# Kernel tuning notes

Hardware: AMD Instinct MI355X
Metric: run time of the kernel (lower is better)

Reference implementation:

```python
import jax, jax.numpy as jnp
import numpy as np

BATCH = 4
N_MELS, T_LEN, PATCH = 128, 512, 16
D_MODEL, D_INNER, D_STATE, DT_RANK, D_CONV = 512, 1024, 16, 32, 4
DEPTH, N_CLASSES = 4, 10


def _silu(x):
    return x * jax.nn.sigmoid(x)


def _ln(x, w, b):
    m = x.mean(-1, keepdims=True)
    v = ((x - m) ** 2).mean(-1, keepdims=True)
    return (x - m) * jax.lax.rsqrt(v + 1e-5) * w + b


def _causal_conv(x, w, b):
    # x: (B, L, D); w: (D, K) depthwise causal conv (mamba conv1d)
    K, L = w.shape[-1], x.shape[1]
    xp = jnp.pad(x, ((0, 0), (K - 1, 0), (0, 0)))
    y = sum(xp[:, k:k + L, :] * w[:, k] for k in range(K))
    return y + b


def _ssm(xc, conv_w, conv_b, xproj_w, dtproj_w, dtproj_b, A_log, Dp):
    # One directional selective scan (mamba S6).
    u = _silu(_causal_conv(xc, conv_w, conv_b))              # (B,L,Di)
    xdbl = jnp.einsum('bld,ed->ble', u, xproj_w)             # (B,L,dt_rank+2S)
    dtr, Bm, Cm = jnp.split(xdbl, [DT_RANK, DT_RANK + D_STATE], axis=-1)
    dt = jax.nn.softplus(jnp.einsum('blr,dr->bld', dtr, dtproj_w) + dtproj_b)
    A = -jnp.exp(A_log)                                      # (Di,S)
    dA = jnp.exp(dt[..., None] * A)                          # (B,L,Di,S)
    dBu = (dt * u)[..., None] * Bm[:, :, None, :]            # (B,L,Di,S)

    def comb(e1, e2):
        a1, b1 = e1
        a2, b2 = e2
        return a1 * a2, a2 * b1 + b2

    _, h = jax.lax.associative_scan(comb, (dA, dBu), axis=1)  # parallel linear recurrence
    return jnp.einsum('blds,bls->bld', h, Cm) + u * Dp


def _forward(x, patch_w, patch_b, in_proj_w, conv_w_f, conv_b_f, conv_w_b, conv_b_b,
             xproj_w_f, xproj_w_b, dtproj_w_f, dtproj_b_f, dtproj_w_b, dtproj_b_b,
             A_log_f, A_log_b, D_f, D_b, out_proj_w, norm_w, norm_b,
             normf_w, normf_b, ln_w, ln_b, fc1_w, fc1_b, fc2_w, fc2_b):
    B = x.shape[0]
    # Patch embed: conv with kernel == stride -> reshape + einsum
    xp = x.reshape(B, 1, N_MELS // PATCH, PATCH, T_LEN // PATCH, PATCH)
    tok = jnp.einsum('bchpwq,dcpq->bhwd', xp, patch_w) + patch_b
    h = tok.reshape(B, -1, D_MODEL)                           # (B, 256, D)
    for i in range(DEPTH):
        xn = _ln(h, norm_w[i], norm_b[i])
        xz = jnp.einsum('bld,ed->ble', xn, in_proj_w[i])
        xc, z = jnp.split(xz, 2, axis=-1)
        y_f = _ssm(xc, conv_w_f[i], conv_b_f[i], xproj_w_f[i],
                   dtproj_w_f[i], dtproj_b_f[i], A_log_f[i], D_f[i])
        y_b = jnp.flip(_ssm(jnp.flip(xc, 1), conv_w_b[i], conv_b_b[i], xproj_w_b[i],
                            dtproj_w_b[i], dtproj_b_b[i], A_log_b[i], D_b[i]), 1)
        y = (y_f + y_b) * _silu(z)                            # bimamba v2: fwd + flipped bwd, gated
        h = h + jnp.einsum('bld,ed->ble', y, out_proj_w[i])
    h = _ln(h, normf_w, normf_b)
    feat = h.mean(axis=1)                                     # pooled features (B, D)
    c = _ln(feat, ln_w, ln_b)
    c = jnp.maximum(c @ fc1_w.T + fc1_b, 0.0)
    return c @ fc2_w.T + fc2_b


def setup_inputs() -> dict:
    ks = iter(jax.random.split(jax.random.key(0), 64))

    def rn(shape, s=0.02):
        return jax.random.normal(next(ks), shape, jnp.float32) * s

    inp = {}
    inp['x'] = jax.random.normal(next(ks), (BATCH, 1, N_MELS, T_LEN), jnp.float32)
    inp['patch_w'] = rn((D_MODEL, 1, PATCH, PATCH))
    inp['patch_b'] = jnp.zeros((D_MODEL,), jnp.float32)
    inp['in_proj_w'] = rn((DEPTH, 2 * D_INNER, D_MODEL))
    A_init = jnp.log(jnp.tile(jnp.arange(1, D_STATE + 1, dtype=jnp.float32), (DEPTH, D_INNER, 1)))
    for sfx in ('f', 'b'):
        inp[f'conv_w_{sfx}'] = rn((DEPTH, D_INNER, D_CONV), 0.2)
        inp[f'conv_b_{sfx}'] = jnp.zeros((DEPTH, D_INNER), jnp.float32)
        inp[f'xproj_w_{sfx}'] = rn((DEPTH, DT_RANK + 2 * D_STATE, D_INNER))
        inp[f'dtproj_w_{sfx}'] = rn((DEPTH, D_INNER, DT_RANK), 0.1)
        inp[f'dtproj_b_{sfx}'] = jnp.full((DEPTH, D_INNER), -4.6, jnp.float32)  # softplus -> dt ~ 0.01
        inp[f'A_log_{sfx}'] = A_init
        inp[f'D_{sfx}'] = jnp.ones((DEPTH, D_INNER), jnp.float32)
    inp['out_proj_w'] = rn((DEPTH, D_MODEL, D_INNER))
    inp['norm_w'] = jnp.ones((DEPTH, D_MODEL), jnp.float32)
    inp['norm_b'] = jnp.zeros((DEPTH, D_MODEL), jnp.float32)
    inp['normf_w'] = jnp.ones((D_MODEL,), jnp.float32)
    inp['normf_b'] = jnp.zeros((D_MODEL,), jnp.float32)
    inp['ln_w'] = jnp.ones((D_MODEL,), jnp.float32)
    inp['ln_b'] = jnp.zeros((D_MODEL,), jnp.float32)
    inp['fc1_w'] = rn((512, D_MODEL))
    inp['fc1_b'] = jnp.zeros((512,), jnp.float32)
    inp['fc2_w'] = rn((N_CLASSES, 512))
    inp['fc2_b'] = jnp.zeros((N_CLASSES,), jnp.float32)
    return inp


def reference(x, patch_w, patch_b, in_proj_w, conv_w_f, conv_b_f, conv_w_b, conv_b_b,
              xproj_w_f, xproj_w_b, dtproj_w_f, dtproj_b_f, dtproj_w_b, dtproj_b_b,
              A_log_f, A_log_b, D_f, D_b, out_proj_w, norm_w, norm_b,
              normf_w, normf_b, ln_w, ln_b, fc1_w, fc1_b, fc2_w, fc2_b):
    return _forward(x, patch_w, patch_b, in_proj_w, conv_w_f, conv_b_f, conv_w_b, conv_b_b,
                    xproj_w_f, xproj_w_b, dtproj_w_f, dtproj_b_f, dtproj_w_b, dtproj_b_b,
                    A_log_f, A_log_b, D_f, D_b, out_proj_w, norm_w, norm_b,
                    normf_w, normf_b, ln_w, ln_b, fc1_w, fc1_b, fc2_w, fc2_b)
```

## Files before the change

kernel.cpp:

```cpp
#include <hip/hip_runtime.h>


#define BB 4
#define LL 256
#define DM 512
#define DI 1024
#define LDST 40

typedef unsigned short u16;
typedef unsigned int u32;
typedef __attribute__((ext_vector_type(8))) short s8v;
typedef __attribute__((ext_vector_type(4))) float f4v;

__device__ __forceinline__ float silu_f(float x){ return x/(1.f+__expf(-x)); }
__device__ __forceinline__ float b2f(u16 u){
  union { u32 i; float f; } v; v.i = ((u32)u) << 16; return v.f;
}
__device__ __forceinline__ u16 f2bf(float f){
  union { float f; u32 u; } v; v.f = f;
  u32 r = (v.u + 0x7fffu + ((v.u >> 16) & 1u)) >> 16;
  return (u16)r;
}

__device__ __forceinline__ float row_sum16(float p){
  union { float f; int i; } v, r;
  v.f = p;
  r.i = __builtin_amdgcn_update_dpp(0, v.i, 0x111, 0xF, 0xF, true); v.f += r.f;
  r.i = __builtin_amdgcn_update_dpp(0, v.i, 0x112, 0xF, 0xF, true); v.f += r.f;
  r.i = __builtin_amdgcn_update_dpp(0, v.i, 0x114, 0xF, 0xF, true); v.f += r.f;
  r.i = __builtin_amdgcn_update_dpp(0, v.i, 0x118, 0xF, 0xF, true); v.f += r.f;
  return v.f;
}

__device__ __forceinline__ void block_reduce2(float& a, float& b, float* sc, int nw){
  int lane = threadIdx.x & 63, wid = threadIdx.x >> 6;
#pragma unroll
  for (int o = 32; o > 0; o >>= 1){
    a += __shfl_down(a, o, 64);
    b += __shfl_down(b, o, 64);
  }
  if (lane == 0){ sc[wid*2] = a; sc[wid*2+1] = b; }
  __syncthreads();
  float ta = 0.f, tb = 0.f;
  for (int i = 0; i < nw; ++i){ ta += sc[i*2]; tb += sc[i*2+1]; }
  a = ta; b = tb;
}

__global__ __launch_bounds__(256) void convert_w(const float* __restrict__ inW,
    const float* __restrict__ outW, u16* __restrict__ inHi, u16* __restrict__ inLo,
    u16* __restrict__ outHi, u16* __restrict__ outLo){
  int idx = blockIdx.x*256 + threadIdx.x;
  const float4* src; ushort4* dh; ushort4* dl;
  if (idx < 262144){
    src = (const float4*)inW + idx;
    dh = (ushort4*)inHi + idx; dl = (ushort4*)inLo + idx;
  } else {
    int j = idx - 262144;
    src = (const float4*)outW + j;
    dh = (ushort4*)outHi + j; dl = (ushort4*)outLo + j;
  }
  float4 v = *src;
  ushort4 h, l;
  h.x = f2bf(v.x); l.x = f2bf(v.x - b2f(h.x));
  h.y = f2bf(v.y); l.y = f2bf(v.y - b2f(h.y));
  h.z = f2bf(v.z); l.z = f2bf(v.z - b2f(h.z));
  h.w = f2bf(v.w); l.w = f2bf(v.w - b2f(h.w));
  *dh = h; *dl = l;
}

__global__ __launch_bounds__(256) void patch_embed(const float* __restrict__ x,
    const float* __restrict__ pw, const float* __restrict__ pb, float* __restrict__ h){
  __shared__ float xs[8*256];
  int blk = blockIdx.x;
  int b = blk >> 6, ph = (blk >> 3) & 7, pg = (blk >> 1) & 3, dh = blk & 1;
  int t = threadIdx.x;
  for (int idx = t; idx < 2048; idx += 256){
    int j = idx >> 8, pix = idx & 255, p = pix >> 4, q = pix & 15;
    xs[idx] = x[(size_t)(b*128 + ph*16 + p)*512 + pg*128 + j*16 + q];
  }
  __syncthreads();
  int d = dh*256 + t;
  float acc[8] = {};
  const float* wr = pw + (size_t)d*256;
  for (int i = 0; i < 256; i += 8){
    float4 w0 = *(const float4*)(wr + i);
    float4 w1 = *(const float4*)(wr + i + 4);
    float wf[8] = {w0.x,w0.y,w0.z,w0.w,w1.x,w1.y,w1.z,w1.w};
#pragma unroll
    for (int j = 0; j < 8; ++j){
#pragma unroll
      for (int jj = 0; jj < 8; ++jj)
        acc[j] = fmaf(xs[j*256 + i + jj], wf[jj], acc[j]);
    }
  }
  float bias = pb[d];
#pragma unroll
  for (int j = 0; j < 8; ++j)
    h[(size_t)(b*256 + ph*32 + pg*8 + j)*512 + d] = acc[j] + bias;
}

__global__ __launch_bounds__(256) void prep_ln(const float* __restrict__ x,
    const float* __restrict__ w, const float* __restrict__ bias, int wOff,
    u16* __restrict__ hiO, u16* __restrict__ loO){
  __shared__ float sc[8];
  int row = blockIdx.x, t = threadIdx.x;
  const float* xr = x + (size_t)row*DM;
  float v0 = xr[t], v1 = xr[t + 256];
  float s = v0 + v1, ss = v0*v0 + v1*v1;
  block_reduce2(s, ss, sc, 4);
  float mean = s * (1.f/512.f);
  float var = ss * (1.f/512.f) - mean*mean;
  float inv = rsqrtf(var + 1e-5f);
  float o0 = (v0 - mean)*inv*w[wOff + t]       + bias[wOff + t];
  float o1 = (v1 - mean)*inv*w[wOff + t + 256] + bias[wOff + t + 256];
  u16 h0 = f2bf(o0), h1 = f2bf(o1);
  hiO[(size_t)row*DM + t]       = h0;
  hiO[(size_t)row*DM + t + 256] = h1;
  loO[(size_t)row*DM + t]       = f2bf(o0 - b2f(h0));
  loO[(size_t)row*DM + t + 256] = f2bf(o1 - b2f(h1));
}

__global__ __launch_bounds__(256) void prep_gate(const float* __restrict__ ybuf,
    const float* __restrict__ xz, u16* __restrict__ gHi, u16* __restrict__ gLo){
  int row = blockIdx.x, t = threadIdx.x;
  int c = t*4;
  float4 yf = *(const float4*)(ybuf + (size_t)row*DI + c);
  float4 yb = *(const float4*)(ybuf + 1048576 + (size_t)row*DI + c);
  float4 zv = *(const float4*)(xz + (size_t)row*2048 + 1024 + c);
  float g0 = (yf.x + yb.x)*silu_f(zv.x);
  float g1 = (yf.y + yb.y)*silu_f(zv.y);
  float g2 = (yf.z + yb.z)*silu_f(zv.z);
  float g3 = (yf.w + yb.w)*silu_f(zv.w);
  ushort4 h, l;
  h.x = f2bf(g0); l.x = f2bf(g0 - b2f(h.x));
  h.y = f2bf(g1); l.y = f2bf(g1 - b2f(h.y));
  h.z = f2bf(g2); l.z = f2bf(g2 - b2f(h.z));
  h.w = f2bf(g3); l.w = f2bf(g3 - b2f(h.w));
  *(ushort4*)(gHi + (size_t)row*DI + c) = h;
  *(ushort4*)(gLo + (size_t)row*DI + c) = l;
}

__global__ __launch_bounds__(256) void gemm_bf16(const u16* __restrict__ Ahi_g,
    const u16* __restrict__ Alo_g, int As, const u16* __restrict__ Bhi_g,
    const u16* __restrict__ Blo_g, int Bs, float* __restrict__ C, int Cs,
    int K, int addFlag){
  __shared__ __align__(16) u16 Ah[64*LDST], Al[64*LDST], Bh[64*LDST], Bl[64*LDST];
  int bm = blockIdx.y*64, bn = blockIdx.x*64;
  int t = threadIdx.x;
  int sr = t >> 2, sc8 = (t & 3)*8;
  int lane = t & 63, wv = t >> 6, ml = lane & 15, quad = lane >> 4;
  int mq = wv >> 1, nq = wv & 1;
  f4v acc[2][2] = {};
  for (int k0 = 0; k0 < K; k0 += 32){
    *(uint4*)&Ah[sr*LDST + sc8] = *(const uint4*)(Ahi_g + (size_t)(bm + sr)*As + k0 + sc8);
    *(uint4*)&Al[sr*LDST + sc8] = *(const uint4*)(Alo_g + (size_t)(bm + sr)*As + k0 + sc8);
    *(uint4*)&Bh[sr*LDST + sc8] = *(const uint4*)(Bhi_g + (size_t)(bn + sr)*Bs + k0 + sc8);
    *(uint4*)&Bl[sr*LDST + sc8] = *(const uint4*)(Blo_g + (size_t)(bn + sr)*Bs + k0 + sc8);
    __syncthreads();
    s8v ah[2], al2[2], bh2[2], bl2[2];
#pragma unroll
    for (int mt = 0; mt < 2; ++mt){
      int row = mq*32 + mt*16 + ml;
      ah[mt]  = *(s8v*)&Ah[row*LDST + quad*8];
      al2[mt] = *(s8v*)&Al[row*LDST + quad*8];
    }
#pragma unroll
    for (int nt = 0; nt < 2; ++nt){
      int col = nq*32 + nt*16 + ml;
      bh2[nt] = *(s8v*)&Bh[col*LDST + quad*8];
      bl2[nt] = *(s8v*)&Bl[col*LDST + quad*8];
    }
#pragma unroll
    for (int mt = 0; mt < 2; ++mt)
#pragma unroll
      for (int nt = 0; nt < 2; ++nt){
        acc[mt][nt] = __builtin_amdgcn_mfma_f32_16x16x32_bf16(ah[mt],  bh2[nt], acc[mt][nt], 0, 0, 0);
        acc[mt][nt] = __builtin_amdgcn_mfma_f32_16x16x32_bf16(al2[mt], bh2[nt], acc[mt][nt], 0, 0, 0);
        acc[mt][nt] = __builtin_amdgcn_mfma_f32_16x16x32_bf16(ah[mt],  bl2[nt], acc[mt][nt], 0, 0, 0);
      }
    __syncthreads();
  }
#pragma unroll
  for (int mt = 0; mt < 2; ++mt)
#pragma unroll
    for (int nt = 0; nt < 2; ++nt)
#pragma unroll
      for (int r = 0; r < 4; ++r){
        float* cp = C + (size_t)(bm + mq*32 + mt*16 + quad*4 + r)*Cs +
                    bn + nq*32 + nt*16 + ml;
        if (addFlag) *cp += acc[mt][nt][r];
        else         *cp  = acc[mt][nt][r];
      }
}

__global__ __launch_bounds__(256) void fused_cxd(const float* __restrict__ xz,
    const float* __restrict__ cwF, const float* __restrict__ cbF,
    const float* __restrict__ cwB, const float* __restrict__ cbB,
    const float* __restrict__ xwF, const float* __restrict__ xwB,
    const float* __restrict__ dtwF, const float* __restrict__ dtbF,
    const float* __restrict__ dtwB, const float* __restrict__ dtbB,
    int cwOff, int cbOff, int xwOff, int dtwOff, int dtbOff,
    float* __restrict__ u, float* __restrict__ xdbl, float* __restrict__ dtout){
  __shared__ float us[4*1024];
  __shared__ float part[16*64];
  __shared__ float dtr[4*32];
  int blk = blockIdx.x;
  int dir = blk >> 8, rem = blk & 255, b = rem >> 6, lg = rem & 63;
  int l0 = lg*4;
  const float* cw  = dir ? cwB  : cwF;
  const float* cb  = dir ? cbB  : cbF;
  const float* xw  = dir ? xwB  : xwF;
  const float* dtw = dir ? dtwB : dtwF;
  const float* dtb = dir ? dtbB : dtbF;
  int t = threadIdx.x;
  int rbase = (dir*BB + b)*LL;
  for (int dd = 0; dd < 4; ++dd){
    int d = t + dd*256;
    float4 w4 = *(const float4*)(cw + cwOff + d*4);
    float wf[4] = {w4.x, w4.y, w4.z, w4.w};
    float bias = cb[cbOff + d];
#pragma unroll
    for (int r = 0; r < 4; ++r){
      int l = l0 + r;
      float acc = bias;
#pragma unroll
      for (int k = 0; k < 4; ++k){
        int li = l + k - 3;
        if (li >= 0){
          int sl = dir ? (LL-1-li) : li;
          acc = fmaf(xz[(size_t)(b*LL + sl)*2048 + d], wf[k], acc);
        }
      }
      float uval = silu_f(acc);
      us[r*1024 + d] = uval;
      u[(size_t)(rbase + l)*DI + d] = uval;
    }
  }
  __syncthreads();
  {
    int e = t & 63, pr = t >> 6;
    float accs[4] = {};
    const float* wr = xw + xwOff + (size_t)e*1024 + pr*256;
    for (int i = 0; i < 256; i += 8){
      float4 w0 = *(const float4*)(wr + i);
      float4 w1 = *(const float4*)(wr + i + 4);
      float wf[8] = {w0.x,w0.y,w0.z,w0.w,w1.x,w1.y,w1.z,w1.w};
#pragma unroll
      for (int r = 0; r < 4; ++r){
        const float* ub = us + r*1024 + pr*256 + i;
#pragma unroll
        for (int j = 0; j < 8; ++j)
          accs[r] = fmaf(ub[j], wf[j], accs[r]);
      }
    }
#pragma unroll
    for (int r = 0; r < 4; ++r) part[(pr*4 + r)*64 + e] = accs[r];
  }
  __syncthreads();
  {
    int r = t >> 6, e = t & 63;
    float v = part[(0*4+r)*64+e] + part[(1*4+r)*64+e] +
              part[(2*4+r)*64+e] + part[(3*4+r)*64+e];
    xdbl[(size_t)(rbase + l0 + r)*64 + e] = v;
    if (e < 32) dtr[r*32 + e] = v;
  }
  __syncthreads();
  for (int dd = 0; dd < 4; ++dd){
    int d = t + dd*256;
    float bias = dtb[dtbOff + d];
    float accs[4] = {bias, bias, bias, bias};
    const float* wr = dtw + dtwOff + (size_t)d*32;
    for (int i = 0; i < 32; i += 8){
      float4 w0 = *(const float4*)(wr + i);
      float4 w1 = *(const float4*)(wr + i + 4);
      float wf[8] = {w0.x,w0.y,w0.z,w0.w,w1.x,w1.y,w1.z,w1.w};
#pragma unroll
      for (int r = 0; r < 4; ++r)
#pragma unroll
        for (int j = 0; j < 8; ++j)
          accs[r] = fmaf(dtr[r*32 + i + j], wf[j], accs[r]);
    }
#pragma unroll
    for (int r = 0; r < 4; ++r){
      float sv = accs[r];
      dtout[(size_t)(rbase + l0 + r)*DI + d] = (sv > 15.f) ? sv : log1pf(__expf(sv));
    }
  }
}

__global__ __launch_bounds__(256) void scan_coal(const float* __restrict__ dt,
    const float* __restrict__ u, const float* __restrict__ xd,
    const float* __restrict__ AlogF, const float* __restrict__ AlogB,
    const float* __restrict__ DF, const float* __restrict__ DB,
    int aOff, int dOff, float* __restrict__ y){
  __shared__ __align__(16) float dtuT[16][516];
  __shared__ __align__(16) float BCT[16][516];
  __shared__ __align__(16) float ytile[128][16];
  int blk = blockIdx.x;
  int dir = blk >> 8, b = (blk >> 6) & 3, dg = blk & 63;
  int t = threadIdx.x;
  int rbase = (dir*BB + b)*LL;
  const float* Alog = dir ? AlogB : AlogF;
  const float* Dpt  = dir ? DB : DF;
  {
    int q = t & 3, lb = t >> 2;
    for (int pass = 0; pass < 4; ++pass){
      int l = pass*64 + lb;
      float4 dv = *(const float4*)(dt + (size_t)(rbase + l)*DI + dg*16 + q*4);
      float4 uv = *(const float4*)(u  + (size_t)(rbase + l)*DI + dg*16 + q*4);
      float2 p0 = {dv.x, uv.x}, p1 = {dv.y, uv.y}, p2 = {dv.z, uv.z}, p3 = {dv.w, uv.w};
      *(float2*)&dtuT[q*4+0][l*2] = p0;
      *(float2*)&dtuT[q*4+1][l*2] = p1;
      *(float2*)&dtuT[q*4+2][l*2] = p2;
      *(float2*)&dtuT[q*4+3][l*2] = p3;
    }
  }
  {
    int h8 = t & 7, lb = t >> 3;
    for (int pass = 0; pass < 8; ++pass){
      int l = pass*32 + lb;
      float4 v = *(const float4*)(xd + (size_t)(rbase + l)*64 + 32 + h8*4);
      if (h8 < 4){
        int s0 = h8*4;
        BCT[s0+0][l*2] = v.x; BCT[s0+1][l*2] = v.y;
        BCT[s0+2][l*2] = v.z; BCT[s0+3][l*2] = v.w;
      } else {
        int s0 = (h8-4)*4;
        BCT[s0+0][l*2+1] = v.x; BCT[s0+1][l*2+1] = v.y;
        BCT[s0+2][l*2+1] = v.z; BCT[s0+3][l*2+1] = v.w;
      }
    }
  }
  int s = t & 15, dl = t >> 4;
  float Av = -__expf(Alog[aOff + dg*256 + t]);
  float Dp = Dpt[dOff + dg*16 + dl];
  __syncthreads();
  float h = 0.f;
  for (int half = 0; half < 2; ++half){
    for (int l0 = half*128; l0 < half*128 + 128; l0 += 4){
      float4 du01 = *(const float4*)&dtuT[dl][l0*2];
      float4 du23 = *(const float4*)&dtuT[dl][l0*2 + 4];
      float4 bc01 = *(const float4*)&BCT[s][l0*2];
      float4 bc23 = *(const float4*)&BCT[s][l0*2 + 4];
      float dtv[4] = {du01.x, du01.z, du23.x, du23.z};
      float uv[4]  = {du01.y, du01.w, du23.y, du23.w};
      float Bv[4]  = {bc01.x, bc01.z, bc23.x, bc23.z};
      float Cv[4]  = {bc01.y, bc01.w, bc23.y, bc23.w};
#pragma unroll
      for (int i = 0; i < 4; ++i){
        float a = __expf(dtv[i] * Av);
        h = fmaf(a, h, dtv[i]*uv[i]*Bv[i]);
        float p = h * Cv[i];
        float sum = row_sum16(p);
        if (s == 15){
          int lr = (l0 + i) & 127;
          ytile[lr][dl] = fmaf(uv[i], Dp, sum);
        }
      }
    }
    __syncthreads();
    {
      int d4 = t & 3, lh = t >> 2;
      for (int pass = 0; pass < 2; ++pass){
        int lr = pass*64 + lh;
        int l = half*128 + lr;
        int lo = dir ? (255 - l) : l;
        float4 vv = *(const float4*)&ytile[lr][d4*4];
        *(float4*)(y + (size_t)(rbase + lo)*DI + dg*16 + d4*4) = vv;
      }
    }
    __syncthreads();
  }
}

__global__ __launch_bounds__(256) void ln_kernel(const float* __restrict__ x,
    const float* __restrict__ w, const float* __restrict__ bias,
    float* __restrict__ y){
  __shared__ float sc[8];
  int row = blockIdx.x, t = threadIdx.x;
  const float* xr = x + (size_t)row*DM;
  float v0 = xr[t], v1 = xr[t + 256];
  float s = v0 + v1, ss = v0*v0 + v1*v1;
  block_reduce2(s, ss, sc, 4);
  float mean = s * (1.f/512.f);
  float var = ss * (1.f/512.f) - mean*mean;
  float inv = rsqrtf(var + 1e-5f);
  float* yr = y + (size_t)row*DM;
  yr[t]       = (v0 - mean)*inv*w[t]       + bias[t];
  yr[t + 256] = (v1 - mean)*inv*w[t + 256] + bias[t + 256];
}

__global__ __launch_bounds__(256) void pool_kernel(const float* __restrict__ hn,
    float* __restrict__ feat){
  __shared__ float part[4][64];
  int b = blockIdx.x >> 3, dg = blockIdx.x & 7;
  int t = threadIdx.x, dl = t & 63, lq = t >> 6;
  const float* p = hn + (size_t)(b*256 + lq*64)*512 + dg*64 + dl;
  float s = 0.f;
#pragma unroll 4
  for (int i = 0; i < 64; ++i) s += p[(size_t)i*512];
  part[lq][dl] = s;
  __syncthreads();
  if (t < 64)
    feat[b*512 + dg*64 + t] =
        (part[0][t] + part[1][t] + part[2][t] + part[3][t]) * (1.f/256.f);
}

__global__ __launch_bounds__(512) void head_kernel(const float* __restrict__ feat,
    const float* __restrict__ lnw, const float* __restrict__ lnb,
    const float* __restrict__ fc1w, const float* __restrict__ fc1b,
    const float* __restrict__ fc2w, const float* __restrict__ fc2b,
    float* __restrict__ out){
  __shared__ float sc[16];
  __shared__ float cbuf[512];
  __shared__ float rbuf[512];
  int b = blockIdx.x, t = threadIdx.x;
  float v = feat[b*512 + t];
  float s = v, ss = v*v;
  block_reduce2(s, ss, sc, 8);
  float mean = s * (1.f/512.f);
  float var = ss * (1.f/512.f) - mean*mean;
  float inv = rsqrtf(var + 1e-5f);
  cbuf[t] = (v - mean)*inv*lnw[t] + lnb[t];
  __syncthreads();
  float a = fc1b[t];
  const float* w1 = fc1w + (size_t)t*512;
  for (int i = 0; i < 512; i += 8){
    float4 w0 = *(const float4*)(w1 + i);
    float4 w4 = *(const float4*)(w1 + i + 4);
    float wf[8] = {w0.x,w0.y,w0.z,w0.w,w4.x,w4.y,w4.z,w4.w};
#pragma unroll
    for (int j = 0; j < 8; ++j) a = fmaf(cbuf[i + j], wf[j], a);
  }
  rbuf[t] = fmaxf(a, 0.f);
  __syncthreads();
  if (t < 10){
    float a2 = fc2b[t];
    const float* w2 = fc2w + (size_t)t*512;
    for (int i = 0; i < 512; ++i) a2 = fmaf(rbuf[i], w2[i], a2);
    out[b*10 + t] = a2;
  }
}

extern "C" void kernel_launch(void* const* d_in, const int* in_sizes, int n_in,
                              void* d_out, int out_size, void* d_ws, size_t ws_size,
                              hipStream_t stream) {
  (void)in_sizes; (void)n_in; (void)out_size; (void)ws_size;
  const float* x          = (const float*)d_in[0];
  const float* patch_w    = (const float*)d_in[1];
  const float* patch_b    = (const float*)d_in[2];
  const float* in_proj_w  = (const float*)d_in[3];
  const float* conv_w_f   = (const float*)d_in[4];
  const float* conv_b_f   = (const float*)d_in[5];
  const float* xproj_w_f  = (const float*)d_in[6];
  const float* dtproj_w_f = (const float*)d_in[7];
  const float* dtproj_b_f = (const float*)d_in[8];
  const float* A_log_f    = (const float*)d_in[9];
  const float* D_f        = (const float*)d_in[10];
  const float* conv_w_b   = (const float*)d_in[11];
  const float* conv_b_b   = (const float*)d_in[12];
  const float* xproj_w_b  = (const float*)d_in[13];
  const float* dtproj_w_b = (const float*)d_in[14];
  const float* dtproj_b_b = (const float*)d_in[15];
  const float* A_log_b    = (const float*)d_in[16];
  const float* D_b        = (const float*)d_in[17];
  const float* out_proj_w = (const float*)d_in[18];
  const float* norm_w     = (const float*)d_in[19];
  const float* norm_b     = (const float*)d_in[20];
  const float* normf_w    = (const float*)d_in[21];
  const float* normf_b    = (const float*)d_in[22];
  const float* ln_w       = (const float*)d_in[23];
  const float* ln_b       = (const float*)d_in[24];
  const float* fc1_w      = (const float*)d_in[25];
  const float* fc1_b      = (const float*)d_in[26];
  const float* fc2_w      = (const float*)d_in[27];
  const float* fc2_b      = (const float*)d_in[28];

  float* ws   = (float*)d_ws;
  float* hbuf = ws;
  float* xz   = ws + 524288;
  float* ubuf = ws + 2621440;
  float* xdbl = ws + 4718592;
  float* dtb  = ws + 4849664;
  float* ybuf = ws + 6946816;
  float* hn   = ws + 9043968;
  u16*   inHi = (u16*)(ws + 9568256);
  u16*   inLo = (u16*)(ws + 10092544);
  u16*   outHi= (u16*)(ws + 10616832);
  u16*   outLo= (u16*)(ws + 10878976);
  float* feat = ws + 11141120;
  u16*   xnHi = (u16*)hn;
  u16*   xnLo = (u16*)(ws + 9043968 + 262144);
  u16*   gHi  = (u16*)ubuf;
  u16*   gLo  = (u16*)(ws + 2621440 + 524288);

  patch_embed<<<256, 256, 0, stream>>>(x, patch_w, patch_b, hbuf);
  for (int i = 0; i < 4; ++i){
    convert_w<<<1536, 256, 0, stream>>>(in_proj_w + (size_t)i*1048576,
                                        out_proj_w + (size_t)i*524288,
                                        inHi, inLo, outHi, outLo);
    prep_ln<<<1024, 256, 0, stream>>>(hbuf, norm_w, norm_b, i*512, xnHi, xnLo);
    gemm_bf16<<<dim3(32, 16), 256, 0, stream>>>(
        xnHi, xnLo, 512, inHi, inLo, 512, xz, 2048, 512, 0);
    fused_cxd<<<512, 256, 0, stream>>>(
        xz, conv_w_f, conv_b_f, conv_w_b, conv_b_b, xproj_w_f, xproj_w_b,
        dtproj_w_f, dtproj_b_f, dtproj_w_b, dtproj_b_b,
        i*4096, i*1024, i*65536, i*32768, i*1024, ubuf, xdbl, dtb);
    scan_coal<<<512, 256, 0, stream>>>(
        dtb, ubuf, xdbl, A_log_f, A_log_b, D_f, D_b, i*16384, i*1024, ybuf);
    prep_gate<<<1024, 256, 0, stream>>>(ybuf, xz, gHi, gLo);
    gemm_bf16<<<dim3(8, 16), 256, 0, stream>>>(
        gHi, gLo, 1024, outHi, outLo, 1024, hbuf, 512, 1024, 1);
  }
  ln_kernel<<<1024, 256, 0, stream>>>(hbuf, normf_w, normf_b, hn);
  pool_kernel<<<32, 256, 0, stream>>>(hn, feat);
  head_kernel<<<4, 512, 0, stream>>>(feat, ln_w, ln_b, fc1_w, fc1_b, fc2_w, fc2_b,
                                     (float*)d_out);
}
```

Baseline: 664.2 us.

## Split fused conv/xproj/dtproj into conv kernel plus split-bf16 MFMA GEMMs

The fused kernel that did the conv, x_proj and dt_proj with scalar fp32 FMAs is split into three kernels: a conv+SiLU kernel and two MFMA GEMMs. The conv kernel writes u as bf16 hi/lo pairs, and both GEMMs use three bf16 MFMA passes per tile (hi·hi, lo·hi, hi·lo) to stay close to fp32 accuracy. The x_proj and dt_proj weights are now converted to hi/lo each layer inside convert_w. The scan kernel rebuilds u from the hi/lo pair. The x_proj GEMM launches only 32 blocks, each looping serially over K=1024, and the split adds two kernel launches per layer. Together these could limit or cancel the benefit of moving the work onto the matrix units.

```diff
diff --git a/kernel.cpp b/kernel.cpp
--- a/kernel.cpp
+++ b/kernel.cpp
@@ -15,6 +15,11 @@
 __device__ __forceinline__ float silu_f(float x){ return x/(1.f+__expf(-x)); }
 __device__ __forceinline__ float b2f(u16 u){
   union { u32 i; float f; } v; v.i = ((u32)u) << 16; return v.f;
+}
+__device__ __forceinline__ void b2x2(u32 w, float& lo, float& hi){
+  union { u32 i; float f; } a, b;
+  a.i = w << 16; b.i = w & 0xffff0000u;
+  lo = a.f; hi = b.f;
 }
 __device__ __forceinline__ u16 f2bf(float f){
   union { float f; u32 u; } v; v.f = f;
@@ -47,17 +52,36 @@
 }
 
 __global__ __launch_bounds__(256) void convert_w(const float* __restrict__ inW,
-    const float* __restrict__ outW, u16* __restrict__ inHi, u16* __restrict__ inLo,
-    u16* __restrict__ outHi, u16* __restrict__ outLo){
+    const float* __restrict__ outW, const float* __restrict__ xwF,
+    const float* __restrict__ xwB, const float* __restrict__ dtwF,
+    const float* __restrict__ dtwB, u16* __restrict__ inHi, u16* __restrict__ inLo,
+    u16* __restrict__ outHi, u16* __restrict__ outLo, u16* __restrict__ xwHi,
+    u16* __restrict__ xwLo, u16* __restrict__ dtwHi, u16* __restrict__ dtwLo){
   int idx = blockIdx.x*256 + threadIdx.x;
   const float4* src; ushort4* dh; ushort4* dl;
   if (idx < 262144){
     src = (const float4*)inW + idx;
     dh = (ushort4*)inHi + idx; dl = (ushort4*)inLo + idx;
-  } else {
+  } else if (idx < 393216){
     int j = idx - 262144;
     src = (const float4*)outW + j;
     dh = (ushort4*)outHi + j; dl = (ushort4*)outLo + j;
+  } else if (idx < 409600){
+    int j = idx - 393216;
+    src = (const float4*)xwF + j;
+    dh = (ushort4*)xwHi + j; dl = (ushort4*)xwLo + j;
+  } else if (idx < 425984){
+    int j = idx - 409600;
+    src = (const float4*)xwB + j;
+    dh = (ushort4*)(xwHi + 65536) + j; dl = (ushort4*)(xwLo + 65536) + j;
+  } else if (idx < 434176){
+    int j = idx - 425984;
+    src = (const float4*)dtwF + j;
+    dh = (ushort4*)dtwHi + j; dl = (ushort4*)dtwLo + j;
+  } else {
+    int j = idx - 434176;
+    src = (const float4*)dtwB + j;
+    dh = (ushort4*)(dtwHi + 32768) + j; dl = (ushort4*)(dtwLo + 32768) + j;
   }
   float4 v = *src;
   ushort4 h, l;
@@ -193,25 +217,15 @@
       }
 }
 
-__global__ __launch_bounds__(256) void fused_cxd(const float* __restrict__ xz,
+__global__ __launch_bounds__(256) void conv_silu_split(const float* __restrict__ xz,
     const float* __restrict__ cwF, const float* __restrict__ cbF,
     const float* __restrict__ cwB, const float* __restrict__ cbB,
-    const float* __restrict__ xwF, const float* __restrict__ xwB,
-    const float* __restrict__ dtwF, const float* __restrict__ dtbF,
-    const float* __restrict__ dtwB, const float* __restrict__ dtbB,
-    int cwOff, int cbOff, int xwOff, int dtwOff, int dtbOff,
-    float* __restrict__ u, float* __restrict__ xdbl, float* __restrict__ dtout){
-  __shared__ float us[4*1024];
-  __shared__ float part[16*64];
-  __shared__ float dtr[4*32];
+    int cwOff, int cbOff, u16* __restrict__ uHi, u16* __restrict__ uLo){
   int blk = blockIdx.x;
   int dir = blk >> 8, rem = blk & 255, b = rem >> 6, lg = rem & 63;
   int l0 = lg*4;
-  const float* cw  = dir ? cwB  : cwF;
-  const float* cb  = dir ? cbB  : cbF;
-  const float* xw  = dir ? xwB  : xwF;
-  const float* dtw = dir ? dtwB : dtwF;
-  const float* dtb = dir ? dtbB : dtbF;
+  const float* cw = dir ? cwB : cwF;
+  const float* cb = dir ? cbB : cbF;
   int t = threadIdx.x;
   int rbase = (dir*BB + b)*LL;
   for (int dd = 0; dd < 4; ++dd){
@@ -232,64 +246,134 @@
         }
       }
       float uval = silu_f(acc);
-      us[r*1024 + d] = uval;
-      u[(size_t)(rbase + l)*DI + d] = uval;
-    }
-  }
+      u16 h = f2bf(uval);
+      uHi[(size_t)(rbase + l)*DI + d] = h;
+      uLo[(size_t)(rbase + l)*DI + d] = f2bf(uval - b2f(h));
+    }
+  }
+}
+
+__global__ __launch_bounds__(256) void gemm_xproj(const u16* __restrict__ uHi,
+    const u16* __restrict__ uLo, const u16* __restrict__ xwHi,
+    const u16* __restrict__ xwLo, float* __restrict__ xdbl,
+    u16* __restrict__ dtrHi, u16* __restrict__ dtrLo){
+  __shared__ __align__(16) u16 Ah[64*LDST], Al[64*LDST], Bh[64*LDST], Bl[64*LDST];
+  int bm = blockIdx.y*64;
+  int dir = bm >> 10;
+  const u16* BhG = xwHi + dir*65536;
+  const u16* BlG = xwLo + dir*65536;
+  int t = threadIdx.x;
+  int sr = t >> 2, sc8 = (t & 3)*8;
+  int lane = t & 63, wv = t >> 6, ml = lane & 15, quad = lane >> 4;
+  int mq = wv >> 1, nq = wv & 1;
+  f4v acc[2][2] = {};
+  for (int k0 = 0; k0 < 1024; k0 += 32){
+    *(uint4*)&Ah[sr*LDST + sc8] = *(const uint4*)(uHi + (size_t)(bm + sr)*1024 + k0 + sc8);
+    *(uint4*)&Al[sr*LDST + sc8] = *(const uint4*)(uLo + (size_t)(bm + sr)*1024 + k0 + sc8);
+    *(uint4*)&Bh[sr*LDST + sc8] = *(const uint4*)(BhG + (size_t)sr*1024 + k0 + sc8);
+    *(uint4*)&Bl[sr*LDST + sc8] = *(const uint4*)(BlG + (size_t)sr*1024 + k0 + sc8);
+    __syncthreads();
+    s8v ah[2], al2[2], bh2[2], bl2[2];
+#pragma unroll
+    for (int mt = 0; mt < 2; ++mt){
+      int row = mq*32 + mt*16 + ml;
+      ah[mt]  = *(s8v*)&Ah[row*LDST + quad*8];
+      al2[mt] = *(s8v*)&Al[row*LDST + quad*8];
+    }
+#pragma unroll
+    for (int nt = 0; nt < 2; ++nt){
+      int col = nq*32 + nt*16 + ml;
+      bh2[nt] = *(s8v*)&Bh[col*LDST + quad*8];
+      bl2[nt] = *(s8v*)&Bl[col*LDST + quad*8];
+    }
+#pragma unroll
+    for (int mt = 0; mt < 2; ++mt)
+#pragma unroll
+      for (int nt = 0; nt < 2; ++nt){
+        acc[mt][nt] = __builtin_amdgcn_mfma_f32_16x16x32_bf16(ah[mt],  bh2[nt], acc[mt][nt], 0, 0, 0);
+        acc[mt][nt] = __builtin_amdgcn_mfma_f32_16x16x32_bf16(al2[mt], bh2[nt], acc[mt][nt], 0, 0, 0);
+        acc[mt][nt] = __builtin_amdgcn_mfma_f32_16x16x32_bf16(ah[mt],  bl2[nt], acc[mt][nt], 0, 0, 0);
+      }
+    __syncthreads();
+  }
+#pragma unroll
+  for (int mt = 0; mt < 2; ++mt)
+#pragma unroll
+    for (int nt = 0; nt < 2; ++nt){
+      int col = nq*32 + nt*16 + ml;
+#pragma unroll
+      for (int r = 0; r < 4; ++r){
+        int row = bm + mq*32 + mt*16 + quad*4 + r;
+        float v = acc[mt][nt][r];
+        xdbl[(size_t)row*64 + col] = v;
+        if (nq == 0){
+          u16 h = f2bf(v);
+          dtrHi[(size_t)row*32 + col] = h;
+          dtrLo[(size_t)row*32 + col] = f2bf(v - b2f(h));
+        }
+      }
+    }
+}
+
+__global__ __launch_bounds__(256) void gemm_dt(const u16* __restrict__ dtrHi,
+    const u16* __restrict__ dtrLo, const u16* __restrict__ dtwHi,
+    const u16* __restrict__ dtwLo, const float* __restrict__ dtbF,
+    const float* __restrict__ dtbB, int bOff, float* __restrict__ dtOut){
+  __shared__ __align__(16) u16 Ah[64*LDST], Al[64*LDST], Bh[64*LDST], Bl[64*LDST];
+  int bm = blockIdx.y*64, bn = blockIdx.x*64;
+  int dir = bm >> 10;
+  const u16* BhG = dtwHi + dir*32768;
+  const u16* BlG = dtwLo + dir*32768;
+  const float* dtb = dir ? dtbB : dtbF;
+  int t = threadIdx.x;
+  int sr = t >> 2, sc8 = (t & 3)*8;
+  int lane = t & 63, wv = t >> 6, ml = lane & 15, quad = lane >> 4;
+  int mq = wv >> 1, nq = wv & 1;
+  *(uint4*)&Ah[sr*LDST + sc8] = *(const uint4*)(dtrHi + (size_t)(bm + sr)*32 + sc8);
+  *(uint4*)&Al[sr*LDST + sc8] = *(const uint4*)(dtrLo + (size_t)(bm + sr)*32 + sc8);
+  *(uint4*)&Bh[sr*LDST + sc8] = *(const uint4*)(BhG + (size_t)(bn + sr)*32 + sc8);
+  *(uint4*)&Bl[sr*LDST + sc8] = *(const uint4*)(BlG + (size_t)(bn + sr)*32 + sc8);
   __syncthreads();
-  {
-    int e = t & 63, pr = t >> 6;
-    float accs[4] = {};
-    const float* wr = xw + xwOff + (size_t)e*1024 + pr*256;
-    for (int i = 0; i < 256; i += 8){
-      float4 w0 = *(const float4*)(wr + i);
-      float4 w1 = *(const float4*)(wr + i + 4);
-      float wf[8] = {w0.x,w0.y,w0.z,w0.w,w1.x,w1.y,w1.z,w1.w};
+  f4v acc[2][2] = {};
+  s8v ah[2], al2[2], bh2[2], bl2[2];
+#pragma unroll
+  for (int mt = 0; mt < 2; ++mt){
+    int row = mq*32 + mt*16 + ml;
+    ah[mt]  = *(s8v*)&Ah[row*LDST + quad*8];
+    al2[mt] = *(s8v*)&Al[row*LDST + quad*8];
+  }
+#pragma unroll
+  for (int nt = 0; nt < 2; ++nt){
+    int col = nq*32 + nt*16 + ml;
+    bh2[nt] = *(s8v*)&Bh[col*LDST + quad*8];
+    bl2[nt] = *(s8v*)&Bl[col*LDST + quad*8];
+  }
+#pragma unroll
+  for (int mt = 0; mt < 2; ++mt)
+#pragma unroll
+    for (int nt = 0; nt < 2; ++nt){
+      acc[mt][nt] = __builtin_amdgcn_mfma_f32_16x16x32_bf16(ah[mt],  bh2[nt], acc[mt][nt], 0, 0, 0);
+      acc[mt][nt] = __builtin_amdgcn_mfma_f32_16x16x32_bf16(al2[mt], bh2[nt], acc[mt][nt], 0, 0, 0);
+      acc[mt][nt] = __builtin_amdgcn_mfma_f32_16x16x32_bf16(ah[mt],  bl2[nt], acc[mt][nt], 0, 0, 0);
+    }
+#pragma unroll
+  for (int mt = 0; mt < 2; ++mt)
+#pragma unroll
+    for (int nt = 0; nt < 2; ++nt){
+      int col = bn + nq*32 + nt*16 + ml;
+      float bias = dtb[bOff + col];
 #pragma unroll
       for (int r = 0; r < 4; ++r){
-        const float* ub = us + r*1024 + pr*256 + i;
-#pragma unroll
-        for (int j = 0; j < 8; ++j)
-          accs[r] = fmaf(ub[j], wf[j], accs[r]);
-      }
-    }
-#pragma unroll
-    for (int r = 0; r < 4; ++r) part[(pr*4 + r)*64 + e] = accs[r];
-  }
-  __syncthreads();
-  {
-    int r = t >> 6, e = t & 63;
-    float v = part[(0*4+r)*64+e] + part[(1*4+r)*64+e] +
-              part[(2*4+r)*64+e] + part[(3*4+r)*64+e];
-    xdbl[(size_t)(rbase + l0 + r)*64 + e] = v;
-    if (e < 32) dtr[r*32 + e] = v;
-  }
-  __syncthreads();
-  for (int dd = 0; dd < 4; ++dd){
-    int d = t + dd*256;
-    float bias = dtb[dtbOff + d];
-    float accs[4] = {bias, bias, bias, bias};
-    const float* wr = dtw + dtwOff + (size_t)d*32;
-    for (int i = 0; i < 32; i += 8){
-      float4 w0 = *(const float4*)(wr + i);
-      float4 w1 = *(const float4*)(wr + i + 4);
-      float wf[8] = {w0.x,w0.y,w0.z,w0.w,w1.x,w1.y,w1.z,w1.w};
-#pragma unroll
-      for (int r = 0; r < 4; ++r)
-#pragma unroll
-        for (int j = 0; j < 8; ++j)
-          accs[r] = fmaf(dtr[r*32 + i + j], wf[j], accs[r]);
-    }
-#pragma unroll
-    for (int r = 0; r < 4; ++r){
-      float sv = accs[r];
-      dtout[(size_t)(rbase + l0 + r)*DI + d] = (sv > 15.f) ? sv : log1pf(__expf(sv));
-    }
-  }
+        int row = bm + mq*32 + mt*16 + quad*4 + r;
+        float sv = acc[mt][nt][r] + bias;
+        dtOut[(size_t)row*1024 + col] = (sv > 15.f) ? sv : log1pf(__expf(sv));
+      }
+    }
 }
 
 __global__ __launch_bounds__(256) void scan_coal(const float* __restrict__ dt,
-    const float* __restrict__ u, const float* __restrict__ xd,
+    const u16* __restrict__ uHi, const u16* __restrict__ uLo,
+    const float* __restrict__ xd,
     const float* __restrict__ AlogF, const float* __restrict__ AlogB,
     const float* __restrict__ DF, const float* __restrict__ DB,
     int aOff, int dOff, float* __restrict__ y){
@@ -306,9 +390,15 @@
     int q = t & 3, lb = t >> 2;
     for (int pass = 0; pass < 4; ++pass){
       int l = pass*64 + lb;
-      float4 dv = *(const float4*)(dt + (size_t)(rbase + l)*DI + dg*16 + q*4);
-      float4 uv = *(const float4*)(u  + (size_t)(rbase + l)*DI + dg*16 + q*4);
-      float2 p0 = {dv.x, uv.x}, p1 = {dv.y, uv.y}, p2 = {dv.z, uv.z}, p3 = {dv.w, uv.w};
+      size_t base = (size_t)(rbase + l)*DI + dg*16 + q*4;
+      float4 dv = *(const float4*)(dt + base);
+      uint2 uh = *(const uint2*)(uHi + base);
+      uint2 ul = *(const uint2*)(uLo + base);
+      float h0,h1,h2,h3,l0f,l1f,l2f,l3f;
+      b2x2(uh.x, h0, h1); b2x2(uh.y, h2, h3);
+      b2x2(ul.x, l0f, l1f); b2x2(ul.y, l2f, l3f);
+      float2 p0 = {dv.x, h0 + l0f}, p1 = {dv.y, h1 + l1f};
+      float2 p2 = {dv.z, h2 + l2f}, p3 = {dv.w, h3 + l3f};
       *(float2*)&dtuT[q*4+0][l*2] = p0;
       *(float2*)&dtuT[q*4+1][l*2] = p1;
       *(float2*)&dtuT[q*4+2][l*2] = p2;
@@ -479,10 +569,17 @@
   float* ws   = (float*)d_ws;
   float* hbuf = ws;
   float* xz   = ws + 524288;
-  float* ubuf = ws + 2621440;
+  u16*   uHi  = (u16*)(ws + 2621440);
+  u16*   uLo  = (u16*)(ws + 2621440 + 1048576);
   float* xdbl = ws + 4718592;
-  float* dtb  = ws + 4849664;
+  float* dtbuf= ws + 4849664;
   float* ybuf = ws + 6946816;
+  u16*   xwHi = (u16*)(ws + 6946816);
+  u16*   xwLo = (u16*)(ws + 7012352);
+  u16*   dtwHi= (u16*)(ws + 7077888);
+  u16*   dtwLo= (u16*)(ws + 7110656);
+  u16*   dtrHi= (u16*)(ws + 7143424);
+  u16*   dtrLo= (u16*)(ws + 7176192);
   float* hn   = ws + 9043968;
   u16*   inHi = (u16*)(ws + 9568256);
   u16*   inLo = (u16*)(ws + 10092544);
@@ -491,23 +588,27 @@
   float* feat = ws + 11141120;
   u16*   xnHi = (u16*)hn;
   u16*   xnLo = (u16*)(ws + 9043968 + 262144);
-  u16*   gHi  = (u16*)ubuf;
+  u16*   gHi  = (u16*)(ws + 2621440);
   u16*   gLo  = (u16*)(ws + 2621440 + 524288);
 
   patch_embed<<<256, 256, 0, stream>>>(x, patch_w, patch_b, hbuf);
   for (int i = 0; i < 4; ++i){
-    convert_w<<<1536, 256, 0, stream>>>(in_proj_w + (size_t)i*1048576,
-                                        out_proj_w + (size_t)i*524288,
-                                        inHi, inLo, outHi, outLo);
+    convert_w<<<1728, 256, 0, stream>>>(
+        in_proj_w + (size_t)i*1048576, out_proj_w + (size_t)i*524288,
+        xproj_w_f + (size_t)i*65536, xproj_w_b + (size_t)i*65536,
+        dtproj_w_f + (size_t)i*32768, dtproj_w_b + (size_t)i*32768,
+        inHi, inLo, outHi, outLo, xwHi, xwLo, dtwHi, dtwLo);
     prep_ln<<<1024, 256, 0, stream>>>(hbuf, norm_w, norm_b, i*512, xnHi, xnLo);
     gemm_bf16<<<dim3(32, 16), 256, 0, stream>>>(
         xnHi, xnLo, 512, inHi, inLo, 512, xz, 2048, 512, 0);
-    fused_cxd<<<512, 256, 0, stream>>>(
-        xz, conv_w_f, conv_b_f, conv_w_b, conv_b_b, xproj_w_f, xproj_w_b,
-        dtproj_w_f, dtproj_b_f, dtproj_w_b, dtproj_b_b,
-        i*4096, i*1024, i*65536, i*32768, i*1024, ubuf, xdbl, dtb);
+    conv_silu_split<<<512, 256, 0, stream>>>(
+        xz, conv_w_f, conv_b_f, conv_w_b, conv_b_b, i*4096, i*1024, uHi, uLo);
+    gemm_xproj<<<dim3(1, 32), 256, 0, stream>>>(
+        uHi, uLo, xwHi, xwLo, xdbl, dtrHi, dtrLo);
+    gemm_dt<<<dim3(16, 32), 256, 0, stream>>>(
+        dtrHi, dtrLo, dtwHi, dtwLo, dtproj_b_f, dtproj_b_b, i*1024, dtbuf);
     scan_coal<<<512, 256, 0, stream>>>(
-        dtb, ubuf, xdbl, A_log_f, A_log_b, D_f, D_b, i*16384, i*1024, ybuf);
+        dtbuf, uHi, uLo, xdbl, A_log_f, A_log_b, D_f, D_b, i*16384, i*1024, ybuf);
     prep_gate<<<1024, 256, 0, stream>>>(ybuf, xz, gHi, gLo);
     gemm_bf16<<<dim3(8, 16), 256, 0, stream>>>(
         gHi, gLo, 1024, outHi, outLo, 1024, hbuf, 512, 1024, 1);
```

New measurement: 691.0 us. 1.04x slower.
